# Kernel optimization log

Measured on AMD Instinct MI355X. Metric: run time of the kernel, lower is better.

Reference implementation:

```python
import jax, jax.numpy as jnp
import numpy as np

N, H, W = 2, 96, 96
HL, WL = 48, 48
NCLS = 59


def _bn_params(key, c):
    k1, k2, k3, k4 = jax.random.split(key, 4)
    g = jax.random.uniform(k1, (c,), minval=0.5, maxval=1.5)
    b = jax.random.normal(k2, (c,)) * 0.1
    m = jax.random.normal(k3, (c,)) * 0.1
    v = jax.random.uniform(k4, (c,), minval=0.5, maxval=1.5)
    return jnp.stack([g, b, m, v])  # [4, C]


def _conv_w(key, shape):
    fan_in = shape[1] * shape[2] * shape[3]
    return jax.random.normal(key, shape) / np.sqrt(fan_in)


def setup_inputs() -> dict:
    key = jax.random.key(0)
    ks = jax.random.split(key, 32)
    return {
        "c1": jax.random.normal(ks[0], (N, 256, H, W)),
        "c2": jax.random.normal(ks[1], (N, 512, HL, WL)),
        "x": jax.random.normal(ks[2], (N, 2048, HL, WL)),
        "w_r1": _conv_w(ks[3], (64, 256, 3, 3)), "bn_r1": _bn_params(ks[4], 64),
        "w_r2": _conv_w(ks[5], (64, 64, 3, 3)), "bn_r2": _bn_params(ks[6], 64),
        "w_r3": _conv_w(ks[7], (64, 512, 1, 1)), "bn_r3": _bn_params(ks[8], 64),
        "w_p1": _conv_w(ks[9], (512, 2048, 1, 1)), "bn_p1": _bn_params(ks[10], 512),
        "w_p2": _conv_w(ks[11], (512, 2048, 1, 1)), "bn_p2": _bn_params(ks[12], 512),
        "w_p3": _conv_w(ks[13], (512, 2048, 1, 1)), "bn_p3": _bn_params(ks[14], 512),
        "w_p4": _conv_w(ks[15], (512, 2048, 1, 1)), "bn_p4": _bn_params(ks[16], 512),
        "w_c5": _conv_w(ks[17], (512, 4096, 3, 3)), "bn_c5": _bn_params(ks[18], 512),
        "w_c6": _conv_w(ks[19], (NCLS, 512, 1, 1)),
        "b_c6": jax.random.normal(ks[20], (NCLS,)) * 0.01,
    }


def conv2d(x, w, padding=0, dilation=1):
    return jax.lax.conv_general_dilated(
        x, w, window_strides=(1, 1), padding=[(padding, padding)] * 2,
        rhs_dilation=(dilation, dilation),
        dimension_numbers=("NCHW", "OIHW", "NCHW"))


def bn(x, p, eps=1e-5):
    g, b, m, v = p[0], p[1], p[2], p[3]
    scale = g * jax.lax.rsqrt(v + eps)
    return (x - m[None, :, None, None]) * scale[None, :, None, None] + b[None, :, None, None]


def resize_bilinear_ac(x, oh, ow):
    # bilinear, align_corners=True (matches torch interpolate)
    n, c, h, w = x.shape
    def coords(inp, out):
        if inp == 1 or out == 1:
            return jnp.zeros((out,), jnp.float32)
        return jnp.arange(out, dtype=jnp.float32) * ((inp - 1) / (out - 1))
    ys, xs = coords(h, oh), coords(w, ow)
    y0 = jnp.clip(jnp.floor(ys).astype(jnp.int32), 0, h - 1)
    y1 = jnp.clip(y0 + 1, 0, h - 1)
    wy = (ys - y0)[None, None, :, None]
    x0 = jnp.clip(jnp.floor(xs).astype(jnp.int32), 0, w - 1)
    x1 = jnp.clip(x0 + 1, 0, w - 1)
    wx = (xs - x0)[None, None, :]
    g = x[:, :, y0, :] * (1.0 - wy) + x[:, :, y1, :] * wy  # [n,c,oh,w]
    return g[:, :, :, x0] * (1.0 - wx[:, None]) + g[:, :, :, x1] * wx[:, None]


def unfold3x3_d2(x):
    # torch unfold(kernel=3, dilation=2, padding=2, stride=1) -> [n,c,9,h*w]
    n, c, h, w = x.shape
    p = jnp.pad(x, ((0, 0), (0, 0), (2, 2), (2, 2)))
    pats = jnp.stack([p[:, :, dy:dy + h, dx:dx + w]
                      for dy in (0, 2, 4) for dx in (0, 2, 4)], axis=2)
    return pats.reshape(n, c, 9, h * w)


def adaptive_avg_pool(x, s):
    n, c, h, w = x.shape  # h, w divisible by s here
    return x.reshape(n, c, s, h // s, s, w // s).mean(axis=(3, 5))


def reference(c1, c2, x, w_r1, bn_r1, w_r2, bn_r2, w_r3, bn_r3,
              w_p1, bn_p1, w_p2, bn_p2, w_p3, bn_p3, w_p4, bn_p4,
              w_c5, bn_c5, w_c6, b_c6):
    n, _, h, w = c1.shape
    # refine(c1): two dilated 3x3 convs -> query features [n,64,h,w]
    r = jax.nn.relu(bn(conv2d(c1, w_r1, padding=2, dilation=2), bn_r1))
    r = jax.nn.relu(bn(conv2d(r, w_r2, padding=2, dilation=2), bn_r2))
    # c2 -> upsample -> refine2 (1x1) -> key features [n,64,h,w]
    c2u = resize_bilinear_ac(c2, h, w)
    c2r = jax.nn.relu(bn(conv2d(c2u, w_r3), bn_r3))
    uc2 = unfold3x3_d2(c2r)                       # [n,64,9,hw]
    q = r.reshape(n, 64, h * w)                   # [n,64,hw]
    energy = jnp.einsum("ncp,nckp->npk", q, uc2)  # [n,hw,9]
    att = jax.nn.softmax(energy, axis=-1)
    # conv5 = PyramidPooling + 3x3 conv(4096->512) + BN + ReLU
    xh, xw = x.shape[2], x.shape[3]
    feats = [x]
    for s, wp, bnp in ((1, w_p1, bn_p1), (2, w_p2, bn_p2), (3, w_p3, bn_p3), (6, w_p4, bn_p4)):
        p = jax.nn.relu(bn(conv2d(adaptive_avg_pool(x, s), wp), bnp))
        feats.append(resize_bilinear_ac(p, xh, xw))
    psp = jnp.concatenate(feats, axis=1)          # [n,4096,xh,xw]
    out = jax.nn.relu(bn(conv2d(psp, w_c5, padding=1, dilation=1), bn_c5))  # [n,512,xh,xw]
    out0 = resize_bilinear_ac(out, h, w)          # [n,512,h,w]
    uo = unfold3x3_d2(out0)                       # [n,512,9,hw]
    agg = jnp.einsum("npk,nckp->ncp", att, uo).reshape(n, 512, h, w)
    # conv6: Dropout2d in eval mode = identity, then 1x1 conv with bias
    return conv2d(agg, w_c6) + b_c6[None, :, None, None]
```

## Files before the change

### kernel.cpp

```cpp
#include <hip/hip_runtime.h>
#include <hip/hip_bf16.h>
#include <cstddef>
#include <cstdint>

typedef __hip_bfloat16 hbf;
typedef __bf16 bf16x8 __attribute__((ext_vector_type(8)));
typedef __bf16 bf16x4 __attribute__((ext_vector_type(4)));
typedef float f32x4 __attribute__((ext_vector_type(4)));

#define GLDS(gp, lp) __builtin_amdgcn_global_load_lds( \
    (const __attribute__((address_space(1))) void*)(gp), \
    (__attribute__((address_space(3))) void*)(lp), 16, 0, 0)

__device__ __forceinline__ void bn_coef(const float* __restrict__ p, int C, int c,
                                        float& s, float& t) {
    float g = p[c];
    float b = p[C + c];
    float m = p[2 * C + c];
    float v = p[3 * C + c];
    s = g * rsqrtf(v + 1e-5f);
    t = b - m * s;
}

__global__ void k_fill0(uint32_t* __restrict__ p, int n) {
    int i = blockIdx.x * blockDim.x + threadIdx.x;
    if (i < n) p[i] = 0u;
}

__global__ __launch_bounds__(256) void k_c1trans(const float* __restrict__ x,
                                                 hbf* __restrict__ c1t) {
    __shared__ float tbuf[32][33];
    const int p0 = blockIdx.x * 32, c0 = blockIdx.y * 32, n = blockIdx.z;
    const int tx = threadIdx.x, ty = threadIdx.y;
#pragma unroll
    for (int i = 0; i < 4; ++i) {
        int ci = c0 + ty * 4 + i;
        tbuf[ty * 4 + i][tx] = x[((size_t)(n * 256 + ci)) * 9216 + p0 + tx];
    }
    __syncthreads();
#pragma unroll
    for (int i = 0; i < 4; ++i) {
        int p = p0 + ty * 4 + i;
        int pp = (p / 96 + 2) * 100 + (p % 96) + 2;
        c1t[((size_t)(n * 10000 + pp)) * 256 + c0 + tx] = __float2bfloat16(tbuf[tx][ty * 4 + i]);
    }
}

__global__ __launch_bounds__(256) void k_wsmall(const float* __restrict__ w1,
                                                hbf* __restrict__ wt1,
                                                const float* __restrict__ w2,
                                                hbf* __restrict__ wt2) {
    int b = blockIdx.x;
    if (b < 64) {
        int idx = b * 256 + threadIdx.x;
        int co = idx >> 8, ci = idx & 255;
        const float* s = w1 + ((size_t)(co * 256 + ci)) * 9;
#pragma unroll
        for (int tap = 0; tap < 9; ++tap)
            wt1[((size_t)(tap * 64 + co)) * 256 + ci] = __float2bfloat16(s[tap]);
    } else {
        int idx = (b - 64) * 256 + threadIdx.x;
        int co = idx >> 6, ci = idx & 63;
        const float* s = w2 + ((size_t)(co * 64 + ci)) * 9;
#pragma unroll
        for (int tap = 0; tap < 9; ++tap)
            wt2[((size_t)(tap * 64 + co)) * 64 + ci] = __float2bfloat16(s[tap]);
    }
}

template <int CI>
__global__ __launch_bounds__(256) void k_dconv_mfma(const hbf* __restrict__ wt,
                                                    const hbf* __restrict__ it,
                                                    float* __restrict__ accout) {
    __shared__ hbf As[2][3][64 * 32];
    __shared__ hbf Bs[2][72 * 32];
    const int tid = threadIdx.x;
    const int l = tid & 63, w = tid >> 6;
    const int P0 = blockIdx.x * 64;
    const int g  = blockIdx.y;
    const int r0 = tid >> 2;
    const int swzk = ((tid & 3) ^ ((r0 >> 1) & 3)) * 8;

    const int n_i = P0 / 9216;
    const int pl0 = P0 - n_i * 9216;
    const int pp0 = (pl0 / 96 + 2) * 100 + (pl0 % 96) + 2;
    const ptrdiff_t browbase = (ptrdiff_t)n_i * 10000 + pp0 + (g - 1) * 200 - 2;

    const int wn = w * 16;
    const int pl_lane = pl0 + wn + (l & 15);
    const int jb = ((pl_lane / 96 + 2) * 100 + (pl_lane % 96) + 2) - pp0;
    const int slotA = ((l >> 4) ^ ((l >> 1) & 3)) * 8;

    f32x4 acc[4];
#pragma unroll
    for (int i = 0; i < 4; ++i) acc[i] = {0.f, 0.f, 0.f, 0.f};

    const hbf* gA = wt + ((size_t)(g * 192 + r0)) * CI + swzk;
    const hbf* gB = it + (size_t)(browbase + r0) * CI + swzk;

#define STAGE_D(buf, k0) do {                                                  \
        hbf* ldsA_ = &As[buf][0][0] + w * 512;                                 \
        hbf* ldsB_ = &Bs[buf][0] + w * 512;                                    \
        _Pragma("unroll")                                                      \
        for (int t_ = 0; t_ < 3; ++t_)                                         \
            GLDS(gA + (size_t)t_ * 64 * CI + (k0), ldsA_ + t_ * 2048);         \
        GLDS(gB + (k0), ldsB_);                                                \
        if (tid < 32)                                                          \
            GLDS(gB + (size_t)64 * CI + (k0), &Bs[buf][0] + 2048);             \
    } while (0)

    STAGE_D(0, 0);
    int cur = 0;
#pragma unroll 2
    for (int k0 = 0; k0 < CI; k0 += 32) {
        __syncthreads();
        if (k0 + 32 < CI) STAGE_D(cur ^ 1, k0 + 32);
#pragma unroll
        for (int t = 0; t < 3; ++t) {
            const int brow = jb + 2 * t;
            bf16x8 bfr = *(const bf16x8*)(&Bs[cur][0] + brow * 32 + (((l >> 4) ^ ((brow >> 1) & 3)) * 8));
#pragma unroll
            for (int ti = 0; ti < 4; ++ti) {
                bf16x8 af = *(const bf16x8*)(&As[cur][t][(ti * 16 + (l & 15)) * 32 + slotA]);
                acc[ti] = __builtin_amdgcn_mfma_f32_16x16x32_bf16(af, bfr, acc[ti], 0, 0, 0);
            }
        }
        cur ^= 1;
    }
#undef STAGE_D

    const int px = P0 + wn + (l & 15);
    const int n2 = px / 9216, pl2 = px % 9216;
#pragma unroll
    for (int ti = 0; ti < 4; ++ti) {
        const int mrow = ti * 16 + (l >> 4) * 4;
        float* dst = accout + ((size_t)(n2 * 64 + mrow)) * 9216 + pl2;
#pragma unroll
        for (int r = 0; r < 4; ++r)
            atomicAdd(dst + (size_t)r * 9216, acc[ti][r]);
    }
}

__global__ __launch_bounds__(256) void k_ep_r1(const float* __restrict__ acc,
                                               const float* __restrict__ bnp,
                                               hbf* __restrict__ r1t) {
    const int q = threadIdx.x >> 6;
    const int ln = threadIdx.x & 63;
    const int pi = blockIdx.x * 64 + ln;
    const int n = pi / 9216, pl = pi % 9216;
    const int pp = (pl / 96 + 2) * 100 + (pl % 96) + 2;
    hbf* dst = r1t + ((size_t)(n * 10000 + pp)) * 64 + q * 16;
    const float* src = acc + (size_t)(n * 64 + q * 16) * 9216 + pl;
#pragma unroll
    for (int i = 0; i < 16; ++i) {
        float s, t; bn_coef(bnp, 64, q * 16 + i, s, t);
        dst[i] = __float2bfloat16(fmaxf(fmaf(src[(size_t)i * 9216], s, t), 0.f));
    }
}

__global__ __launch_bounds__(192) void k_conv1x1_c2(const float* __restrict__ c2,
                                                    const float* __restrict__ w,
                                                    float* __restrict__ outacc) {
    const int x = threadIdx.x;
    const int y = blockIdx.y * 4 + threadIdx.y;
    const int n = blockIdx.z >> 2;
    const int ci0 = (blockIdx.z & 3) * 128;
    const int cg = blockIdx.x;
    const int p = y * 48 + x;
    float acc[8];
#pragma unroll
    for (int j = 0; j < 8; ++j) acc[j] = 0.f;
    for (int ci = ci0; ci < ci0 + 128; ++ci) {
        float iv = c2[(size_t)(n * 512 + ci) * 2304 + p];
#pragma unroll
        for (int j = 0; j < 8; ++j)
            acc[j] = fmaf(iv, w[(size_t)(cg * 8 + j) * 512 + ci], acc[j]);
    }
#pragma unroll
    for (int j = 0; j < 8; ++j)
        atomicAdd(&outacc[(size_t)(n * 64 + cg * 8 + j) * 2304 + p], acc[j]);
}

__global__ void k_up96(const float* __restrict__ src, float* __restrict__ dst,
                       int C, const float* __restrict__ bnp) {
    int idx = blockIdx.x * blockDim.x + threadIdx.x;
    int p = idx % 9216;
    int nc = idx / 9216;
    int c = nc % C;
    int y = p / 96, x = p % 96;
    int yn = y * 47, xn = x * 47;
    int y0 = yn / 95, x0 = xn / 95;
    float wy = (float)(yn - y0 * 95) * (1.f / 95.f);
    float wx = (float)(xn - x0 * 95) * (1.f / 95.f);
    int y1 = min(y0 + 1, 47), x1 = min(x0 + 1, 47);
    const float* sp = src + (size_t)nc * 2304;
    float v00 = sp[y0 * 48 + x0], v01 = sp[y0 * 48 + x1];
    float v10 = sp[y1 * 48 + x0], v11 = sp[y1 * 48 + x1];
    float v = (v00 * (1.f - wx) + v01 * wx) * (1.f - wy)
            + (v10 * (1.f - wx) + v11 * wx) * wy;
    if (bnp) {
        float s, t; bn_coef(bnp, C, c, s, t);
        v = fmaxf(fmaf(v, s, t), 0.f);
    }
    dst[idx] = v;
}

__global__ __launch_bounds__(256) void k_attention(const float* __restrict__ qa,
                                                   const float* __restrict__ bnp,
                                                   const float* __restrict__ kf,
                                                   float* __restrict__ att) {
    const int wv = threadIdx.x >> 6;
    const int ln = threadIdx.x & 63;
    const int p_abs = blockIdx.x * 64 + ln;
    const int n = p_abs / 9216, p = p_abs % 9216;
    const int y = p / 96, x = p % 96;
    const float* qb = qa + ((size_t)(n * 64 + wv * 16)) * 9216 + p;
    float qv[16];
#pragma unroll
    for (int c = 0; c < 16; ++c) {
        float s, t; bn_coef(bnp, 64, wv * 16 + c, s, t);
        qv[c] = fmaxf(fmaf(qb[(size_t)c * 9216], s, t), 0.f);
    }
    const float* kb = kf + ((size_t)(n * 64 + wv * 16)) * 9216;
    float e[9];
#pragma unroll
    for (int ky = 0; ky < 3; ++ky)
#pragma unroll
        for (int kx = 0; kx < 3; ++kx) {
            int yy = y + 2 * ky - 2, xx = x + 2 * kx - 2;
            float s = 0.f;
            if (yy >= 0 && yy < 96 && xx >= 0 && xx < 96) {
                const float* kp = kb + yy * 96 + xx;
#pragma unroll
                for (int c = 0; c < 16; ++c) s = fmaf(qv[c], kp[(size_t)c * 9216], s);
            }
            e[ky * 3 + kx] = s;
        }
    __shared__ float pe[9][4][64];
#pragma unroll
    for (int k = 0; k < 9; ++k) pe[k][wv][ln] = e[k];
    __syncthreads();
    if (threadIdx.x < 64) {
        float ee[9];
#pragma unroll
        for (int k = 0; k < 9; ++k)
            ee[k] = (pe[k][0][ln] + pe[k][1][ln]) + (pe[k][2][ln] + pe[k][3][ln]);
        float m = ee[0];
#pragma unroll
        for (int k = 1; k < 9; ++k) m = fmaxf(m, ee[k]);
        float sum = 0.f;
#pragma unroll
        for (int k = 0; k < 9; ++k) { ee[k] = __expf(ee[k] - m); sum += ee[k]; }
        float inv = 1.f / sum;
        float* ap = att + (size_t)p_abs * 9;
#pragma unroll
        for (int k = 0; k < 9; ++k) ap[k] = ee[k] * inv;
    }
}

__global__ __launch_bounds__(64) void k_pool(const float* __restrict__ xin,
                                             float* __restrict__ pooled) {
    int b = blockIdx.x;
    int t = threadIdx.x;
    __shared__ float cells[50];
    if (t < 50) cells[t] = 0.f;
    __syncthreads();
    float rs = 0.f;
    if (t < 48) {
        const f32x4* rowv = (const f32x4*)(xin + (size_t)b * 2304 + t * 48);
        float s6[6];
#pragma unroll
        for (int j = 0; j < 6; ++j) {
            f32x4 u = rowv[2 * j], v = rowv[2 * j + 1];
            s6[j] = ((u[0] + u[1]) + (u[2] + u[3])) + ((v[0] + v[1]) + (v[2] + v[3]));
        }
        float s3a = s6[0] + s6[1], s3b = s6[2] + s6[3], s3c = s6[4] + s6[5];
        float s2a = s3a + s6[2], s2b = s6[3] + s3c;
        rs = s2a + s2b;
        int r6 = t >> 3, r3 = t >> 4, r2 = t / 24;
        atomicAdd(&cells[14 + r6 * 6 + 0], s6[0]);
        atomicAdd(&cells[14 + r6 * 6 + 1], s6[1]);
        atomicAdd(&cells[14 + r6 * 6 + 2], s6[2]);
        atomicAdd(&cells[14 + r6 * 6 + 3], s6[3]);
        atomicAdd(&cells[14 + r6 * 6 + 4], s6[4]);
        atomicAdd(&cells[14 + r6 * 6 + 5], s6[5]);
        atomicAdd(&cells[5 + r3 * 3 + 0], s3a);
        atomicAdd(&cells[5 + r3 * 3 + 1], s3b);
        atomicAdd(&cells[5 + r3 * 3 + 2], s3c);
        atomicAdd(&cells[1 + r2 * 2 + 0], s2a);
        atomicAdd(&cells[1 + r2 * 2 + 1], s2b);
    }
#pragma unroll
    for (int off = 32; off > 0; off >>= 1) rs += __shfl_down(rs, off);
    if (t == 0) atomicAdd(&cells[0], rs);
    __syncthreads();
    if (t < 50) {
        float inv = (t == 0) ? (1.f / 2304.f)
                  : (t < 5)  ? (1.f / 576.f)
                  : (t < 14) ? (1.f / 256.f)
                             : (1.f / 64.f);
        pooled[(size_t)b * 50 + t] = cells[t] * inv;
    }
}

__global__ __launch_bounds__(64) void k_pconv2(const float* __restrict__ pooled,
        const float* __restrict__ wp1, const float* __restrict__ bn1,
        const float* __restrict__ wp2, const float* __restrict__ bn2,
        const float* __restrict__ wp3, const float* __restrict__ bn3,
        const float* __restrict__ wp4, const float* __restrict__ bn4,
        float* __restrict__ pconv) {
    const int co = blockIdx.x, n = blockIdx.y;
    const int t = threadIdx.x;
    const int cell = (t < 50) ? t : 49;
    const float* w; const float* bnp;
    if (cell == 0)      { w = wp1; bnp = bn1; }
    else if (cell < 5)  { w = wp2; bnp = bn2; }
    else if (cell < 14) { w = wp3; bnp = bn3; }
    else                { w = wp4; bnp = bn4; }
    const float* pin = pooled + (size_t)n * 2048 * 50 + cell;
    const float* wr = w + (size_t)co * 2048;
    float a0 = 0.f, a1 = 0.f, a2 = 0.f, a3 = 0.f;
    for (int c = 0; c < 2048; c += 4) {
        a0 = fmaf(pin[(size_t)c * 50],       wr[c],     a0);
        a1 = fmaf(pin[(size_t)(c + 1) * 50], wr[c + 1], a1);
        a2 = fmaf(pin[(size_t)(c + 2) * 50], wr[c + 2], a2);
        a3 = fmaf(pin[(size_t)(c + 3) * 50], wr[c + 3], a3);
    }
    float a = (a0 + a1) + (a2 + a3);
    float s, tt; bn_coef(bnp, 512, co, s, tt);
    if (t < 50)
        pconv[((size_t)n * 512 + co) * 50 + cell] = fmaxf(fmaf(a, s, tt), 0.f);
}

__global__ __launch_bounds__(256) void k_wtrans_all(const float* __restrict__ w5,
                                                    hbf* __restrict__ wt,
                                                    hbf* __restrict__ wpsp) {
    int b = blockIdx.x;
    if (b < 4096) {
        int idx = b * 256 + threadIdx.x;
        int co = idx >> 11, ci = idx & 2047;
        const float* s = w5 + ((size_t)co * 4096 + ci) * 9;
#pragma unroll
        for (int tap = 0; tap < 9; ++tap)
            wt[((size_t)(tap * 512 + co)) * 2048 + ci] = __float2bfloat16(s[tap]);
    } else {
        int r = b - 4096;
        const int co = (r & 7) * 64 + (threadIdx.x & 63);
        const int bb = (r >> 3) & 3;
        const int c0 = (r >> 5) * 64 + (threadIdx.x >> 6) * 16;
        for (int i = 0; i < 16; ++i) {
            int c = c0 + i;
            const float* s = w5 + ((size_t)co * 4096 + 2048 + bb * 512 + c) * 9;
#pragma unroll
            for (int tap = 0; tap < 9; ++tap)
                wpsp[(((size_t)(tap * 4 + bb) * 512) + c) * 512 + co] = __float2bfloat16(s[tap]);
        }
    }
}

__global__ __launch_bounds__(64) void k_computeM2(const hbf* __restrict__ wpsp,
                                                  const float* __restrict__ pconv,
                                                  float* __restrict__ M) {
    const int cog = blockIdx.x, tap = blockIdx.y;
    const int n = blockIdx.z / 7, chunk = blockIdx.z % 7;
    const int cell0_t[7] = {0, 1, 5, 14, 23, 32, 41};
    const int ncell_t[7] = {1, 4, 9, 9, 9, 9, 9};
    const int btab[7]    = {0, 1, 2, 3, 3, 3, 3};
    const int cell0 = cell0_t[chunk], nc = ncell_t[chunk], b = btab[chunk];
    const int co = cog * 64 + threadIdx.x;
    const hbf* wb = wpsp + ((size_t)(tap * 4 + b) * 512) * 512 + co;
    const float* pc = pconv + (size_t)n * 512 * 50 + cell0;
    float acc[9];
#pragma unroll
    for (int j = 0; j < 9; ++j) acc[j] = 0.f;
    for (int c = 0; c < 512; ++c) {
        float w = __bfloat162float(wb[(size_t)c * 512]);
#pragma unroll
        for (int j = 0; j < 9; ++j)
            acc[j] = fmaf(w, pc[c * 50 + j], acc[j]);
    }
    float* Mp = M + ((size_t)(n * 512 + co) * 9 + tap) * 50 + cell0;
    for (int j = 0; j < nc; ++j) Mp[j] = acc[j];
}

struct B4 { int c0, c1, c2, c3; float w0, w1, w2, w3; };
__device__ __forceinline__ B4 cell_interp(int yy, int xx, int s, int base) {
    int sm1 = s - 1;
    int yn = yy * sm1, xn = xx * sm1;
    int y0 = yn / 47, x0 = xn / 47;
    float wy = (float)(yn - y0 * 47) * (1.f / 47.f);
    float wx = (float)(xn - x0 * 47) * (1.f / 47.f);
    int y1 = min(y0 + 1, sm1), x1 = min(x0 + 1, sm1);
    B4 r;
    r.c0 = base + y0 * s + x0; r.c1 = base + y0 * s + x1;
    r.c2 = base + y1 * s + x0; r.c3 = base + y1 * s + x1;
    r.w0 = (1.f - wy) * (1.f - wx); r.w1 = (1.f - wy) * wx;
    r.w2 = wy * (1.f - wx);         r.w3 = wy * wx;
    return r;
}

__global__ __launch_bounds__(256) void k_xtrans(const float* __restrict__ x,
                                                hbf* __restrict__ xtp) {
    __shared__ float tbuf[32][33];
    const int p0 = blockIdx.x * 32, c0 = blockIdx.y * 32, n = blockIdx.z;
    const int tx = threadIdx.x, ty = threadIdx.y;
#pragma unroll
    for (int i = 0; i < 4; ++i) {
        int ci = c0 + ty * 4 + i;
        tbuf[ty * 4 + i][tx] = x[((size_t)(n * 2048 + ci)) * 2304 + p0 + tx];
    }
    __syncthreads();
#pragma unroll
    for (int i = 0; i < 4; ++i) {
        int p = p0 + ty * 4 + i;
        int pp = (p / 48 + 1) * 50 + (p % 48) + 1;
        xtp[((size_t)(n * 2500 + pp)) * 2048 + c0 + tx] = __float2bfloat16(tbuf[tx][ty * 4 + i]);
    }
}

__global__ __launch_bounds__(256) void k_conv5_mfma(const hbf* __restrict__ wt,
                                                    const hbf* __restrict__ xtp,
                                                    float* __restrict__ c5acc) {
    __shared__ hbf As[2][3][128 * 32];
    __shared__ hbf Bs[2][136 * 32];
    const int tid = threadIdx.x;
    const int l = tid & 63, w = tid >> 6;
    const int m0 = blockIdx.x * 128;
    const int P0 = blockIdx.y * 128;
    const int g  = blockIdx.z;
    const int n_img = P0 / 2304;
    const int pbase = P0 - n_img * 2304;
    const int r0 = tid >> 2;
    const int swzk = ((tid & 3) ^ ((r0 >> 1) & 3)) * 8;

    const int pp0 = pbase + 2 * (pbase / 48) + 51;
    const ptrdiff_t browbase = (ptrdiff_t)n_img * 2500 + pp0 + (g - 1) * 50 - 1;

    const int wm = (w & 1) * 64, wn = (w >> 1) * 64;
    int jb[4];
#pragma unroll
    for (int tj = 0; tj < 4; ++tj) {
        int p = pbase + wn + tj * 16 + (l & 15);
        jb[tj] = p + 2 * (p / 48) + 51 - pp0;
    }
    const int slotA = ((l >> 4) ^ ((l >> 1) & 3)) * 8;

    f32x4 acc[4][4];
#pragma unroll
    for (int i = 0; i < 4; ++i)
#pragma unroll
        for (int j = 0; j < 4; ++j) acc[i][j] = {0.f, 0.f, 0.f, 0.f};

    const hbf* gA = wt + ((size_t)(g * 1536 + m0 + r0)) * 2048 + swzk;
    const hbf* gB = xtp + (size_t)(browbase + r0) * 2048 + swzk;

#define STAGE5(buf, k0) do {                                                       \
        hbf* ldsA_ = &As[buf][0][0] + w * 512;                                     \
        hbf* ldsB_ = &Bs[buf][0] + w * 512;                                        \
        _Pragma("unroll")                                                          \
        for (int t_ = 0; t_ < 3; ++t_) {                                           \
            GLDS(gA + (size_t)t_ * 512 * 2048 + (k0),             ldsA_ + t_ * 4096);      \
            GLDS(gA + (size_t)t_ * 512 * 2048 + 64 * 2048 + (k0), ldsA_ + t_ * 4096 + 2048); \
        }                                                                          \
        GLDS(gB + (k0),                      ldsB_);                               \
        GLDS(gB + (size_t)64 * 2048 + (k0),  ldsB_ + 2048);                        \
        if (tid < 32)                                                              \
            GLDS(gB + (size_t)128 * 2048 + (k0), &Bs[buf][0] + 4096);              \
    } while (0)

    STAGE5(0, 0);
    int cur = 0;
#pragma unroll 2
    for (int k0 = 0; k0 < 2048; k0 += 32) {
        __syncthreads();
        if (k0 + 32 < 2048) STAGE5(cur ^ 1, k0 + 32);
        __builtin_amdgcn_s_setprio(1);
#pragma unroll
        for (int t = 0; t < 3; ++t) {
            bf16x8 af[4], bfr[4];
#pragma unroll
            for (int ti = 0; ti < 4; ++ti)
                af[ti] = *(const bf16x8*)(&As[cur][t][(wm + ti * 16 + (l & 15)) * 32 + slotA]);
#pragma unroll
            for (int tj = 0; tj < 4; ++tj) {
                const int brow = jb[tj] + t;
                bfr[tj] = *(const bf16x8*)(&Bs[cur][0] + brow * 32 + (((l >> 4) ^ ((brow >> 1) & 3)) * 8));
            }
#pragma unroll
            for (int ti = 0; ti < 4; ++ti)
#pragma unroll
                for (int tj = 0; tj < 4; ++tj)
                    acc[ti][tj] = __builtin_amdgcn_mfma_f32_16x16x32_bf16(
                        af[ti], bfr[tj], acc[ti][tj], 0, 0, 0);
        }
        __builtin_amdgcn_s_setprio(0);
        cur ^= 1;
    }
#undef STAGE5

#pragma unroll
    for (int ti = 0; ti < 4; ++ti) {
        const int mrow = wm + ti * 16 + (l >> 4) * 4;
#pragma unroll
        for (int tj = 0; tj < 4; ++tj) {
            const int p = pbase + wn + tj * 16 + (l & 15);
            float* dst = c5acc + ((size_t)(n_img * 512 + m0 + mrow)) * 2304 + p;
#pragma unroll
            for (int r = 0; r < 4; ++r)
                atomicAdd(dst + (size_t)r * 2304, acc[ti][tj][r]);
        }
    }
}

__global__ __launch_bounds__(256) void k_bnrelu_psp(const float* __restrict__ c5acc,
                                                    const float* __restrict__ M,
                                                    const float* __restrict__ bnp,
                                                    hbf* __restrict__ c5out) {
    const int co = blockIdx.x, n = blockIdx.y;
    __shared__ float Ms[450];
    const float* Mrow = M + ((size_t)(n * 512 + co)) * 450;
    for (int i = threadIdx.x; i < 450; i += 256) Ms[i] = Mrow[i];
    __syncthreads();
    float s, t; bn_coef(bnp, 512, co, s, t);
    const size_t base = ((size_t)(n * 512 + co)) * 2304;
#pragma unroll
    for (int i = 0; i < 9; ++i) {
        int p = threadIdx.x + i * 256;
        int y = p / 48, x = p % 48;
        float a = c5acc[base + p];
#pragma unroll
        for (int ky = 0; ky < 3; ++ky) {
            int yy = y + ky - 1;
            if (yy < 0 || yy > 47) continue;
#pragma unroll
            for (int kx = 0; kx < 3; ++kx) {
                int xx = x + kx - 1;
                if (xx < 0 || xx > 47) continue;
                const float* Mp = Ms + (ky * 3 + kx) * 50;
                float sa = Mp[0];
                B4 b2 = cell_interp(yy, xx, 2, 1);
                B4 b3 = cell_interp(yy, xx, 3, 5);
                B4 b6 = cell_interp(yy, xx, 6, 14);
                sa = fmaf(b2.w0, Mp[b2.c0], sa); sa = fmaf(b2.w1, Mp[b2.c1], sa);
                sa = fmaf(b2.w2, Mp[b2.c2], sa); sa = fmaf(b2.w3, Mp[b2.c3], sa);
                sa = fmaf(b3.w0, Mp[b3.c0], sa); sa = fmaf(b3.w1, Mp[b3.c1], sa);
                sa = fmaf(b3.w2, Mp[b3.c2], sa); sa = fmaf(b3.w3, Mp[b3.c3], sa);
                sa = fmaf(b6.w0, Mp[b6.c0], sa); sa = fmaf(b6.w1, Mp[b6.c1], sa);
                sa = fmaf(b6.w2, Mp[b6.c2], sa); sa = fmaf(b6.w3, Mp[b6.c3], sa);
                a += sa;
            }
        }
        c5out[base + p] = __float2bfloat16(fmaxf(fmaf(a, s, t), 0.f));
    }
}

__global__ __launch_bounds__(192) void k_conv6s(const hbf* __restrict__ c5o,
                                                const float* __restrict__ w,
                                                float* __restrict__ out) {
    const int p4 = blockIdx.y * 192 + threadIdx.x;
    const int n = blockIdx.z;
    const int co = blockIdx.x;
    const hbf* ip = c5o + (size_t)n * 512 * 2304 + p4 * 4;
    const float* wr = w + (size_t)co * 512;
    float a0 = 0.f, a1 = 0.f, a2 = 0.f, a3 = 0.f;
    for (int ci = 0; ci < 512; ++ci) {
        bf16x4 v = *(const bf16x4*)(ip + (size_t)ci * 2304);
        float wv = wr[ci];
        a0 = fmaf((float)v[0], wv, a0);
        a1 = fmaf((float)v[1], wv, a1);
        a2 = fmaf((float)v[2], wv, a2);
        a3 = fmaf((float)v[3], wv, a3);
    }
    f32x4 res = {a0, a1, a2, a3};
    *(f32x4*)(out + ((size_t)n * 59 + co) * 2304 + p4 * 4) = res;
}

__global__ void k_final(const float* __restrict__ att, const float* __restrict__ c6s,
                        const float* __restrict__ bias, float* __restrict__ out) {
    int idx = blockIdx.x * blockDim.x + threadIdx.x;
    int p = idx % 9216;
    int nc = idx / 9216;
    int cls = nc % 59, n = nc / 59;
    int y = p / 96, x = p % 96;
    const float* ar = att + ((size_t)n * 9216 + p) * 9;
    const float* cp = c6s + (size_t)nc * 2304;
    int xs0[3], xs1[3], ys0[3], ys1[3];
    float fx[3], fy[3];
#pragma unroll
    for (int d = 0; d < 3; ++d) {
        int xx = x + 2 * d - 2;
        if (xx >= 0 && xx < 96) {
            int xn = xx * 47, x0 = xn / 95;
            xs0[d] = x0; xs1[d] = min(x0 + 1, 47);
            fx[d] = (float)(xn - x0 * 95) * (1.f / 95.f);
        } else { xs0[d] = -1; xs1[d] = 0; fx[d] = 0.f; }
        int yy = y + 2 * d - 2;
        if (yy >= 0 && yy < 96) {
            int yn = yy * 47, y0 = yn / 95;
            ys0[d] = y0; ys1[d] = min(y0 + 1, 47);
            fy[d] = (float)(yn - y0 * 95) * (1.f / 95.f);
        } else { ys0[d] = -1; ys1[d] = 0; fy[d] = 0.f; }
    }
    float a = bias[cls];
#pragma unroll
    for (int ky = 0; ky < 3; ++ky) {
        if (ys0[ky] < 0) continue;
        const float* r0 = cp + ys0[ky] * 48;
        const float* r1 = cp + ys1[ky] * 48;
        float wy = fy[ky];
#pragma unroll
        for (int kx = 0; kx < 3; ++kx) {
            if (xs0[kx] < 0) continue;
            float wx = fx[kx];
            float v0 = r0[xs0[kx]] * (1.f - wx) + r0[xs1[kx]] * wx;
            float v1 = r1[xs0[kx]] * (1.f - wx) + r1[xs1[kx]] * wx;
            a = fmaf(ar[ky * 3 + kx], v0 * (1.f - wy) + v1 * wy, a);
        }
    }
    out[idx] = a;
}

extern "C" void kernel_launch(void* const* d_in, const int* in_sizes, int n_in,
                              void* d_out, int out_size, void* d_ws, size_t ws_size,
                              hipStream_t stream) {
    const float* c1    = (const float*)d_in[0];
    const float* c2    = (const float*)d_in[1];
    const float* xin   = (const float*)d_in[2];
    const float* w_r1  = (const float*)d_in[3];
    const float* bn_r1 = (const float*)d_in[4];
    const float* w_r2  = (const float*)d_in[5];
    const float* bn_r2 = (const float*)d_in[6];
    const float* w_r3  = (const float*)d_in[7];
    const float* bn_r3 = (const float*)d_in[8];
    const float* w_p1  = (const float*)d_in[9];
    const float* bn_p1 = (const float*)d_in[10];
    const float* w_p2  = (const float*)d_in[11];
    const float* bn_p2 = (const float*)d_in[12];
    const float* w_p3  = (const float*)d_in[13];
    const float* bn_p3 = (const float*)d_in[14];
    const float* w_p4  = (const float*)d_in[15];
    const float* bn_p4 = (const float*)d_in[16];
    const float* w_c5  = (const float*)d_in[17];
    const float* bn_c5 = (const float*)d_in[18];
    const float* w_c6  = (const float*)d_in[19];
    const float* b_c6  = (const float*)d_in[20];
    float* out = (float*)d_out;
    (void)in_sizes; (void)n_in; (void)out_size; (void)ws_size;

    char* base = (char*)d_ws;
    float* att = (float*)base;
    char*  A   = base + 663552;
    hbf*   c1t   = (hbf*)A;
    hbf*   r1t   = (hbf*)(A + 10240000);
    float* r1acc = (float*)(A + 12800000);
    float* qacc  = (float*)(A + 17518592);
    float* c2acc = (float*)(A + 22237184);
    float* c2r   = (float*)(A + 28135424);
    hbf*   wr1t  = (hbf*)(A + 32854016);
    hbf*   wr2t  = (hbf*)(A + 33148928);
    hbf*   wpsp   = (hbf*)A;
    float* pooled = (float*)(A + 48791552);
    float* pconv  = (float*)(A + 49610752);
    float* M      = (float*)(A + 49815552);
    hbf*   xtp    = (hbf*)A;
    float* c5acc  = (float*)(A + 20480000);
    hbf*   wt     = (hbf*)(A + 29917184);
    hbf*   c5out = (hbf*)A;
    float* c6s   = (float*)(A + 4718592);

    k_fill0<<<dim3(22868), 256, 0, stream>>>((uint32_t*)A, 5854208);
    k_c1trans<<<dim3(288, 8, 2), dim3(32, 8), 0, stream>>>(c1, c1t);
    k_wsmall<<<dim3(80), 256, 0, stream>>>(w_r1, wr1t, w_r2, wr2t);
    k_dconv_mfma<256><<<dim3(288, 3), 256, 0, stream>>>(wr1t, c1t, r1acc);
    k_ep_r1<<<dim3(288), 256, 0, stream>>>(r1acc, bn_r1, r1t);
    k_dconv_mfma<64><<<dim3(288, 3), 256, 0, stream>>>(wr2t, r1t, qacc);
    k_conv1x1_c2<<<dim3(8, 12, 8), dim3(48, 4), 0, stream>>>(c2, w_r3, c2acc);
    k_up96<<<dim3(2 * 64 * 9216 / 256), 256, 0, stream>>>(c2acc, c2r, 64, bn_r3);
    k_attention<<<dim3(288), 256, 0, stream>>>(qacc, bn_r2, c2r, att);
    k_pool<<<dim3(4096), 64, 0, stream>>>(xin, pooled);
    k_pconv2<<<dim3(512, 2), 64, 0, stream>>>(pooled, w_p1, bn_p1, w_p2, bn_p2,
                                              w_p3, bn_p3, w_p4, bn_p4, pconv);
    k_wtrans_all<<<dim3(4352), 256, 0, stream>>>(w_c5, wt, wpsp);
    k_computeM2<<<dim3(8, 9, 14), 64, 0, stream>>>(wpsp, pconv, M);
    k_fill0<<<dim3(29216), 256, 0, stream>>>((uint32_t*)xtp, 7479296);
    k_xtrans<<<dim3(72, 64, 2), dim3(32, 8), 0, stream>>>(xin, xtp);
    k_conv5_mfma<<<dim3(4, 36, 3), 256, 0, stream>>>(wt, xtp, c5acc);
    k_bnrelu_psp<<<dim3(512, 2), 256, 0, stream>>>(c5acc, M, bn_c5, c5out);
    k_conv6s<<<dim3(59, 3, 2), 192, 0, stream>>>(c5out, w_c6, c6s);
    k_final<<<dim3(2 * 59 * 9216 / 256), 256, 0, stream>>>(att, c6s, b_c6, out);
}
```

Baseline: 684.5 us.

## Widen dconv pixel tile, transpose pooled layout, rework conv6s, drop setprio

The dilated-conv MFMA kernel now gives each block 128 pixels instead of 64, with two B fragments per wave, so each A fragment is reused across more MFMAs and half as many atomics-launching blocks are needed. The pooled buffer is stored channel-contiguous so pconv2 can use vectorized float4 loads. conv6s is changed to one output pixel per thread with more blocks. The s_setprio calls around the conv5 MFMA loop are removed. The larger dconv tile raises LDS use and register pressure, and halves the block count, which could lower occupancy.

```diff
diff --git a/kernel.cpp b/kernel.cpp
--- a/kernel.cpp
+++ b/kernel.cpp
@@ -73,10 +73,10 @@
                                                     const hbf* __restrict__ it,
                                                     float* __restrict__ accout) {
     __shared__ hbf As[2][3][64 * 32];
-    __shared__ hbf Bs[2][72 * 32];
+    __shared__ hbf Bs[2][140 * 32];
     const int tid = threadIdx.x;
     const int l = tid & 63, w = tid >> 6;
-    const int P0 = blockIdx.x * 64;
+    const int P0 = blockIdx.x * 128;
     const int g  = blockIdx.y;
     const int r0 = tid >> 2;
     const int swzk = ((tid & 3) ^ ((r0 >> 1) & 3)) * 8;
@@ -86,14 +86,20 @@
     const int pp0 = (pl0 / 96 + 2) * 100 + (pl0 % 96) + 2;
     const ptrdiff_t browbase = (ptrdiff_t)n_i * 10000 + pp0 + (g - 1) * 200 - 2;
 
-    const int wn = w * 16;
-    const int pl_lane = pl0 + wn + (l & 15);
-    const int jb = ((pl_lane / 96 + 2) * 100 + (pl_lane % 96) + 2) - pp0;
+    const int wn = w * 32;
+    int jb[2];
+#pragma unroll
+    for (int tj = 0; tj < 2; ++tj) {
+        int pl_lane = pl0 + wn + tj * 16 + (l & 15);
+        jb[tj] = ((pl_lane / 96 + 2) * 100 + (pl_lane % 96) + 2) - pp0;
+    }
     const int slotA = ((l >> 4) ^ ((l >> 1) & 3)) * 8;
 
-    f32x4 acc[4];
-#pragma unroll
-    for (int i = 0; i < 4; ++i) acc[i] = {0.f, 0.f, 0.f, 0.f};
+    f32x4 acc[4][2];
+#pragma unroll
+    for (int i = 0; i < 4; ++i)
+#pragma unroll
+        for (int j = 0; j < 2; ++j) acc[i][j] = {0.f, 0.f, 0.f, 0.f};
 
     const hbf* gA = wt + ((size_t)(g * 192 + r0)) * CI + swzk;
     const hbf* gB = it + (size_t)(browbase + r0) * CI + swzk;
@@ -105,8 +111,9 @@
         for (int t_ = 0; t_ < 3; ++t_)                                         \
             GLDS(gA + (size_t)t_ * 64 * CI + (k0), ldsA_ + t_ * 2048);         \
         GLDS(gB + (k0), ldsB_);                                                \
-        if (tid < 32)                                                          \
-            GLDS(gB + (size_t)64 * CI + (k0), &Bs[buf][0] + 2048);             \
+        GLDS(gB + (size_t)64 * CI + (k0), ldsB_ + 2048);                       \
+        if (tid < 48)                                                          \
+            GLDS(gB + (size_t)128 * CI + (k0), &Bs[buf][0] + 4096);            \
     } while (0)
 
     STAGE_D(0, 0);
@@ -117,27 +124,38 @@
         if (k0 + 32 < CI) STAGE_D(cur ^ 1, k0 + 32);
 #pragma unroll
         for (int t = 0; t < 3; ++t) {
-            const int brow = jb + 2 * t;
-            bf16x8 bfr = *(const bf16x8*)(&Bs[cur][0] + brow * 32 + (((l >> 4) ^ ((brow >> 1) & 3)) * 8));
-#pragma unroll
-            for (int ti = 0; ti < 4; ++ti) {
-                bf16x8 af = *(const bf16x8*)(&As[cur][t][(ti * 16 + (l & 15)) * 32 + slotA]);
-                acc[ti] = __builtin_amdgcn_mfma_f32_16x16x32_bf16(af, bfr, acc[ti], 0, 0, 0);
+            bf16x8 af[4], bfr[2];
+#pragma unroll
+            for (int ti = 0; ti < 4; ++ti)
+                af[ti] = *(const bf16x8*)(&As[cur][t][(ti * 16 + (l & 15)) * 32 + slotA]);
+#pragma unroll
+            for (int tj = 0; tj < 2; ++tj) {
+                const int brow = jb[tj] + 2 * t;
+                bfr[tj] = *(const bf16x8*)(&Bs[cur][0] + brow * 32 + (((l >> 4) ^ ((brow >> 1) & 3)) * 8));
             }
+#pragma unroll
+            for (int ti = 0; ti < 4; ++ti)
+#pragma unroll
+                for (int tj = 0; tj < 2; ++tj)
+                    acc[ti][tj] = __builtin_amdgcn_mfma_f32_16x16x32_bf16(
+                        af[ti], bfr[tj], acc[ti][tj], 0, 0, 0);
         }
         cur ^= 1;
     }
 #undef STAGE_D
 
-    const int px = P0 + wn + (l & 15);
-    const int n2 = px / 9216, pl2 = px % 9216;
 #pragma unroll
     for (int ti = 0; ti < 4; ++ti) {
         const int mrow = ti * 16 + (l >> 4) * 4;
-        float* dst = accout + ((size_t)(n2 * 64 + mrow)) * 9216 + pl2;
-#pragma unroll
-        for (int r = 0; r < 4; ++r)
-            atomicAdd(dst + (size_t)r * 9216, acc[ti][r]);
+#pragma unroll
+        for (int tj = 0; tj < 2; ++tj) {
+            const int px = P0 + wn + tj * 16 + (l & 15);
+            const int n2 = px / 9216, pl2 = px % 9216;
+            float* dst = accout + ((size_t)(n2 * 64 + mrow)) * 9216 + pl2;
+#pragma unroll
+            for (int r = 0; r < 4; ++r)
+                atomicAdd(dst + (size_t)r * 9216, acc[ti][tj][r]);
+        }
     }
 }
 
@@ -299,11 +317,11 @@
                   : (t < 5)  ? (1.f / 576.f)
                   : (t < 14) ? (1.f / 256.f)
                              : (1.f / 64.f);
-        pooled[(size_t)b * 50 + t] = cells[t] * inv;
-    }
-}
-
-__global__ __launch_bounds__(64) void k_pconv2(const float* __restrict__ pooled,
+        pooled[((size_t)(b >> 11) * 50 + t) * 2048 + (b & 2047)] = cells[t] * inv;
+    }
+}
+
+__global__ __launch_bounds__(64) void k_pconv2(const float* __restrict__ pooled_t,
         const float* __restrict__ wp1, const float* __restrict__ bn1,
         const float* __restrict__ wp2, const float* __restrict__ bn2,
         const float* __restrict__ wp3, const float* __restrict__ bn3,
@@ -317,14 +335,16 @@
     else if (cell < 5)  { w = wp2; bnp = bn2; }
     else if (cell < 14) { w = wp3; bnp = bn3; }
     else                { w = wp4; bnp = bn4; }
-    const float* pin = pooled + (size_t)n * 2048 * 50 + cell;
+    const float* pin = pooled_t + ((size_t)n * 50 + cell) * 2048;
     const float* wr = w + (size_t)co * 2048;
     float a0 = 0.f, a1 = 0.f, a2 = 0.f, a3 = 0.f;
     for (int c = 0; c < 2048; c += 4) {
-        a0 = fmaf(pin[(size_t)c * 50],       wr[c],     a0);
-        a1 = fmaf(pin[(size_t)(c + 1) * 50], wr[c + 1], a1);
-        a2 = fmaf(pin[(size_t)(c + 2) * 50], wr[c + 2], a2);
-        a3 = fmaf(pin[(size_t)(c + 3) * 50], wr[c + 3], a3);
+        f32x4 v = *(const f32x4*)(pin + c);
+        f32x4 ww = *(const f32x4*)(wr + c);
+        a0 = fmaf(v[0], ww[0], a0);
+        a1 = fmaf(v[1], ww[1], a1);
+        a2 = fmaf(v[2], ww[2], a2);
+        a3 = fmaf(v[3], ww[3], a3);
     }
     float a = (a0 + a1) + (a2 + a3);
     float s, tt; bn_coef(bnp, 512, co, s, tt);
@@ -474,7 +494,6 @@
     for (int k0 = 0; k0 < 2048; k0 += 32) {
         __syncthreads();
         if (k0 + 32 < 2048) STAGE5(cur ^ 1, k0 + 32);
-        __builtin_amdgcn_s_setprio(1);
 #pragma unroll
         for (int t = 0; t < 3; ++t) {
             bf16x8 af[4], bfr[4];
@@ -493,7 +512,6 @@
                     acc[ti][tj] = __builtin_amdgcn_mfma_f32_16x16x32_bf16(
                         af[ti], bfr[tj], acc[ti][tj], 0, 0, 0);
         }
-        __builtin_amdgcn_s_setprio(0);
         cur ^= 1;
     }
 #undef STAGE5
@@ -557,22 +575,21 @@
 __global__ __launch_bounds__(192) void k_conv6s(const hbf* __restrict__ c5o,
                                                 const float* __restrict__ w,
                                                 float* __restrict__ out) {
-    const int p4 = blockIdx.y * 192 + threadIdx.x;
+    const int x = threadIdx.x;
+    const int y = blockIdx.y * 4 + threadIdx.y;
     const int n = blockIdx.z;
     const int co = blockIdx.x;
-    const hbf* ip = c5o + (size_t)n * 512 * 2304 + p4 * 4;
+    const int p = y * 48 + x;
+    const hbf* ip = c5o + (size_t)n * 512 * 2304 + p;
     const float* wr = w + (size_t)co * 512;
     float a0 = 0.f, a1 = 0.f, a2 = 0.f, a3 = 0.f;
-    for (int ci = 0; ci < 512; ++ci) {
-        bf16x4 v = *(const bf16x4*)(ip + (size_t)ci * 2304);
-        float wv = wr[ci];
-        a0 = fmaf((float)v[0], wv, a0);
-        a1 = fmaf((float)v[1], wv, a1);
-        a2 = fmaf((float)v[2], wv, a2);
-        a3 = fmaf((float)v[3], wv, a3);
-    }
-    f32x4 res = {a0, a1, a2, a3};
-    *(f32x4*)(out + ((size_t)n * 59 + co) * 2304 + p4 * 4) = res;
+    for (int ci = 0; ci < 512; ci += 4) {
+        a0 = fmaf(__bfloat162float(ip[(size_t)ci * 2304]),       wr[ci],     a0);
+        a1 = fmaf(__bfloat162float(ip[(size_t)(ci + 1) * 2304]), wr[ci + 1], a1);
+        a2 = fmaf(__bfloat162float(ip[(size_t)(ci + 2) * 2304]), wr[ci + 2], a2);
+        a3 = fmaf(__bfloat162float(ip[(size_t)(ci + 3) * 2304]), wr[ci + 3], a3);
+    }
+    out[((size_t)n * 59 + co) * 2304 + p] = (a0 + a1) + (a2 + a3);
 }
 
 __global__ void k_final(const float* __restrict__ att, const float* __restrict__ c6s,
@@ -671,9 +688,9 @@
     k_fill0<<<dim3(22868), 256, 0, stream>>>((uint32_t*)A, 5854208);
     k_c1trans<<<dim3(288, 8, 2), dim3(32, 8), 0, stream>>>(c1, c1t);
     k_wsmall<<<dim3(80), 256, 0, stream>>>(w_r1, wr1t, w_r2, wr2t);
-    k_dconv_mfma<256><<<dim3(288, 3), 256, 0, stream>>>(wr1t, c1t, r1acc);
+    k_dconv_mfma<256><<<dim3(144, 3), 256, 0, stream>>>(wr1t, c1t, r1acc);
     k_ep_r1<<<dim3(288), 256, 0, stream>>>(r1acc, bn_r1, r1t);
-    k_dconv_mfma<64><<<dim3(288, 3), 256, 0, stream>>>(wr2t, r1t, qacc);
+    k_dconv_mfma<64><<<dim3(144, 3), 256, 0, stream>>>(wr2t, r1t, qacc);
     k_conv1x1_c2<<<dim3(8, 12, 8), dim3(48, 4), 0, stream>>>(c2, w_r3, c2acc);
     k_up96<<<dim3(2 * 64 * 9216 / 256), 256, 0, stream>>>(c2acc, c2r, 64, bn_r3);
     k_attention<<<dim3(288), 256, 0, stream>>>(qacc, bn_r2, c2r, att);
@@ -686,6 +703,6 @@
     k_xtrans<<<dim3(72, 64, 2), dim3(32, 8), 0, stream>>>(xin, xtp);
     k_conv5_mfma<<<dim3(4, 36, 3), 256, 0, stream>>>(wt, xtp, c5acc);
     k_bnrelu_psp<<<dim3(512, 2), 256, 0, stream>>>(c5acc, M, bn_c5, c5out);
-    k_conv6s<<<dim3(59, 3, 2), 192, 0, stream>>>(c5out, w_c6, c6s);
+    k_conv6s<<<dim3(59, 12, 2), dim3(48, 4), 0, stream>>>(c5out, w_c6, c6s);
     k_final<<<dim3(2 * 59 * 9216 / 256), 256, 0, stream>>>(att, c6s, b_c6, out);
 }
```

Result: faster. 661.7 us (-3.3%).
